# Kernel tuning notes

Hardware: AMD Instinct MI355X
Metric: run time of the kernel (lower is better)

Reference implementation:

```python
import jax, jax.numpy as jnp
import numpy as np

N = 50000   # nodes (single node type)
E = 200000  # edges per relation
R = 2       # relations (etypes)
D = 256     # in_dim == out_dim
H = 8       # heads
DK = D // H # 32
SQRT_DK = float(np.sqrt(DK))


def setup_inputs() -> dict:
    key = jax.random.key(0)
    ks = jax.random.split(key, 12)
    wsc = 1.0 / np.sqrt(D)   # linear-layer scale
    rsc = 1.0 / np.sqrt(DK)  # xavier-ish scale for relation tensors
    return {
        "x": jax.random.normal(ks[0], (N, D), jnp.float32),
        "src": jax.random.randint(ks[1], (R, E), 0, N, jnp.int32),
        "dst": jax.random.randint(ks[2], (R, E), 0, N, jnp.int32),
        "Wk": jax.random.normal(ks[3], (D, D), jnp.float32) * wsc,
        "bk": jnp.zeros((D,), jnp.float32),
        "Wq": jax.random.normal(ks[4], (D, D), jnp.float32) * wsc,
        "bq": jnp.zeros((D,), jnp.float32),
        "Wv": jax.random.normal(ks[5], (D, D), jnp.float32) * wsc,
        "bv": jnp.zeros((D,), jnp.float32),
        "Wa": jax.random.normal(ks[6], (D, D), jnp.float32) * wsc,
        "ba": jnp.zeros((D,), jnp.float32),
        "rel_pri": jnp.ones((R, H), jnp.float32),
        "rel_att": jax.random.normal(ks[7], (R, H, DK, DK), jnp.float32) * rsc,
        "rel_msg": jax.random.normal(ks[8], (R, H, DK, DK), jnp.float32) * rsc,
        "skip": jnp.ones((1,), jnp.float32),
    }


def reference(x, src, dst, Wk, bk, Wq, bq, Wv, bv, Wa, ba, rel_pri, rel_att, rel_msg, skip):
    # Per-type K/Q/V projections (single node type) -> [N,H,DK]
    k = (x @ Wk + bk).reshape(N, H, DK)
    q = (x @ Wq + bq).reshape(N, H, DK)
    v = (x @ Wv + bv).reshape(N, H, DK)

    # edge_attention: per-relation bmm transform of gathered src features
    key_t = jnp.einsum('rehd,rhdf->rehf', k[src], rel_att)   # [R,E,H,DK]
    val = jnp.einsum('rehd,rhdf->rehf', v[src], rel_msg)     # [R,E,H,DK]
    att = (q[dst] * key_t).sum(-1) * rel_pri[:, None, :] / SQRT_DK  # [R,E,H]

    # segment softmax over incoming edges per (relation, dst node)
    seg = (dst + N * jnp.arange(R, dtype=dst.dtype)[:, None]).reshape(-1)  # [R*E]
    att_f = att.reshape(R * E, H)
    m = jax.ops.segment_max(att_f, seg, num_segments=R * N)
    m = jnp.where(jnp.isfinite(m), m, 0.0)  # empty segments -> never gathered
    e = jnp.exp(att_f - m[seg])
    den = jax.ops.segment_sum(e, seg, num_segments=R * N)
    attn = e / den[seg]                                       # [R*E,H]

    # weighted-sum scatter aggregation, then cross_reducer='mean' over relations
    h = jax.ops.segment_sum(attn[:, :, None] * val.reshape(R * E, H, DK), seg,
                            num_segments=R * N)               # [R*N,H,DK]
    t = h.reshape(R, N, D).mean(axis=0)                        # [N,D]

    # skip-gated output projection (dropout inactive in eval, use_norm=False)
    alpha = jax.nn.sigmoid(skip[0])
    return (t @ Wa + ba) * alpha + x * (1.0 - alpha)
```

## Files before the change

kernel.cpp:

```cpp
#include <hip/hip_runtime.h>
#include <hip/hip_bf16.h>
#include <math.h>

#define NN 50000
#define EE 200000
#define DD 256
#define HH 8
#define DKK 32
#define NSEG (2 * NN)
#define SCAN_BLOCKS ((NSEG + 1023) / 1024)
#define MPAD 50048
#define LDQKV 1280

constexpr float RSQRT_DK = 0.17677669529663687f;

__device__ __forceinline__ float bf_lo(unsigned u) { return __uint_as_float(u << 16); }
__device__ __forceinline__ float bf_hi(unsigned u) { return __uint_as_float(u & 0xffff0000u); }
__device__ __forceinline__ unsigned short f2bf(float f) {
    unsigned u = __float_as_uint(f);
    return (unsigned short)((u + 0x7fffu + ((u >> 16) & 1u)) >> 16);
}

typedef __attribute__((ext_vector_type(8))) short bf16x8;
typedef __attribute__((ext_vector_type(4))) float f32x4;

#define GLDS16(g, l)                                                                   \
    __builtin_amdgcn_global_load_lds((const __attribute__((address_space(1))) unsigned int*)(g), \
                                     (__attribute__((address_space(3))) unsigned int*)(l), 16, 0, 0)

__global__ void cast_x_kernel(const float* __restrict__ x, unsigned short* __restrict__ xb) {
    const size_t i = ((size_t)blockIdx.x * 256 + threadIdx.x) * 4;
    float4 v = *(const float4*)&x[i];
    ushort4 o;
    o.x = f2bf(v.x); o.y = f2bf(v.y); o.z = f2bf(v.z); o.w = f2bf(v.w);
    *(ushort4*)&xb[i] = o;
}

__global__ void fold_qkv_kernel(const float* __restrict__ Wq, const float* __restrict__ Wk,
                                const float* __restrict__ Wv, const float* __restrict__ bq,
                                const float* __restrict__ bk, const float* __restrict__ bv,
                                const float* __restrict__ rel_att, const float* __restrict__ rel_msg,
                                unsigned short* __restrict__ Wt, float* __restrict__ bb) {
    const int n = blockIdx.x, kk = threadIdx.x;
    if (n < 256) {
        Wt[(size_t)n * 256 + kk] = f2bf(Wq[(size_t)kk * 256 + n]);
        if (kk == 0) bb[n] = bq[n];
        return;
    }
    const int sec = (n - 256) >> 8;
    const int c = (n - 256) & 255;
    const int h = c >> 5, f = c & 31;
    const float* W    = (sec < 2) ? Wk : Wv;
    const float* bsrc = (sec < 2) ? bk : bv;
    const float* T = ((sec < 2) ? rel_att : rel_msg)
                   + (size_t)(sec & 1) * HH * DKK * DKK + (size_t)h * DKK * DKK + f;
    const float* wrow = &W[(size_t)kk * 256 + h * 32];
    float s = 0.f;
    #pragma unroll
    for (int d = 0; d < 32; ++d) s += wrow[d] * T[(size_t)d * 32];
    Wt[(size_t)n * 256 + kk] = f2bf(s);
    if (kk == 0) {
        float sb = 0.f;
        for (int d = 0; d < 32; ++d) sb += bsrc[h * 32 + d] * T[(size_t)d * 32];
        bb[n] = sb;
    }
}

__global__ void cast_wa_kernel(const float* __restrict__ Wa, unsigned short* __restrict__ Bt) {
    const int n = blockIdx.x, kk = threadIdx.x;
    Bt[(size_t)n * 256 + kk] = f2bf(Wa[(size_t)kk * 256 + n]);
}

__global__ __launch_bounds__(256) void mfma_gemm(
        const unsigned short* __restrict__ A, const unsigned short* __restrict__ Bt,
        const float* __restrict__ bias,
        unsigned short* __restrict__ Cbf, float* __restrict__ Cf,
        int M, int ldc, const float* __restrict__ xres, const float* __restrict__ skip) {
    __shared__ __align__(16) unsigned short As[3][8][64][8];
    __shared__ __align__(16) unsigned short Bs[3][8][64][8];
    const int t = threadIdx.x;
    const int w = t >> 6, l = t & 63;

    const int nwg = gridDim.x * gridDim.y;
    int lin = blockIdx.y * gridDim.x + blockIdx.x;
    {
        const int xcd = lin & 7, pos = lin >> 3;
        const int q = nwg >> 3, r = nwg & 7;
        lin = (xcd < r ? xcd * (q + 1) : r * (q + 1) + (xcd - r) * q) + pos;
    }
    const int n0 = (lin % gridDim.x) * 128;
    const int m0 = (lin / gridDim.x) * 128;
    const int wm = w & 1, wn = w >> 1;

    const int sr = l & 15, sq = l >> 4;
    const unsigned short* ga0 = A  + (size_t)(m0 + w * 16 + sr) * 256 + sq * 8;
    const unsigned short* ga1 = A  + (size_t)(m0 + (w + 4) * 16 + sr) * 256 + sq * 8;
    const unsigned short* gb0 = Bt + (size_t)(n0 + w * 16 + sr) * 256 + sq * 8;
    const unsigned short* gb1 = Bt + (size_t)(n0 + (w + 4) * 16 + sr) * 256 + sq * 8;

#define STAGE(buf, k0) do {                    \
        GLDS16(ga0 + (k0), &As[buf][w][0][0]); \
        GLDS16(ga1 + (k0), &As[buf][w + 4][0][0]); \
        GLDS16(gb0 + (k0), &Bs[buf][w][0][0]); \
        GLDS16(gb1 + (k0), &Bs[buf][w + 4][0][0]); } while (0)

    f32x4 acc[4][4];
    #pragma unroll
    for (int mi = 0; mi < 4; ++mi)
        #pragma unroll
        for (int ni = 0; ni < 4; ++ni) acc[mi][ni] = (f32x4){0.f, 0.f, 0.f, 0.f};

    STAGE(0, 0);
    STAGE(1, 32);
    #pragma unroll
    for (int it = 0; it < 8; ++it) {
        if (it < 7) { asm volatile("s_waitcnt vmcnt(4)" ::: "memory"); }
        else        { asm volatile("s_waitcnt vmcnt(0)" ::: "memory"); }
        __builtin_amdgcn_s_barrier();
        __builtin_amdgcn_sched_barrier(0);
        if (it < 6) {
            STAGE((it + 2) % 3, (it + 2) * 32);
        }
        const int b = it % 3;
        bf16x8 af[4], bfr[4];
        #pragma unroll
        for (int i = 0; i < 4; ++i) {
            af[i]  = *(const bf16x8*)&As[b][wm * 4 + i][l][0];
            bfr[i] = *(const bf16x8*)&Bs[b][wn * 4 + i][l][0];
        }
        #pragma unroll
        for (int mi = 0; mi < 4; ++mi)
            #pragma unroll
            for (int ni = 0; ni < 4; ++ni)
                acc[mi][ni] = __builtin_amdgcn_mfma_f32_16x16x32_bf16(af[mi], bfr[ni],
                                                                      acc[mi][ni], 0, 0, 0);
    }
    __syncthreads();

    unsigned short* ep = (w < 2) ? &As[0][0][0][0] : &Bs[0][0][0][0];
    ep += (w & 1) * 4096;
    const int q4 = l >> 4, c15 = l & 15;

    if (Cf == nullptr) {
        #pragma unroll
        for (int ni = 0; ni < 4; ++ni) {
            const float bcol = bias[n0 + wn * 64 + ni * 16 + c15];
            const int g = ni * 2 + (c15 >> 3);
            #pragma unroll
            for (int mi = 0; mi < 4; ++mi)
                #pragma unroll
                for (int p = 0; p < 4; ++p) {
                    const int row = mi * 16 + q4 * 4 + p;
                    ep[row * 64 + ((g ^ (row & 7)) << 3) + (c15 & 7)] =
                        f2bf(acc[mi][ni][p] + bcol);
                }
        }
        __syncthreads();
        const int rs = l >> 3, cc = l & 7;
        #pragma unroll
        for (int i = 0; i < 8; ++i) {
            const int rl = i * 8 + rs;
            const int row = m0 + wm * 64 + rl;
            if (row < M) {
                uint4 v = *(const uint4*)&ep[rl * 64 + ((cc ^ (rl & 7)) << 3)];
                *(uint4*)&Cbf[(size_t)row * (size_t)ldc + n0 + wn * 64 + cc * 8] = v;
            }
        }
    } else {
        const float alpha = 1.f / (1.f + __expf(-skip[0]));
        const float beta = 1.f - alpha;
        float* epf = (float*)ep;
        #pragma unroll
        for (int half = 0; half < 2; ++half) {
            __syncthreads();
            #pragma unroll
            for (int mi2 = 0; mi2 < 2; ++mi2) {
                const int mi = half * 2 + mi2;
                #pragma unroll
                for (int ni = 0; ni < 4; ++ni) {
                    const float bcol = bias[n0 + wn * 64 + ni * 16 + c15];
                    const int g = ni * 4 + (c15 >> 2);
                    #pragma unroll
                    for (int p = 0; p < 4; ++p) {
                        const int row = mi2 * 16 + q4 * 4 + p;
                        epf[row * 64 + ((g ^ (row & 7)) << 2) + (c15 & 3)] =
                            acc[mi][ni][p] + bcol;
                    }
                }
            }
            __syncthreads();
            const int cc = l & 15, rs = l >> 4;
            #pragma unroll
            for (int i = 0; i < 8; ++i) {
                const int rl = i * 4 + rs;
                const int row = m0 + wm * 64 + half * 32 + rl;
                if (row < M) {
                    const int col = n0 + wn * 64 + cc * 4;
                    float4 v = *(const float4*)&epf[rl * 64 + ((cc ^ (rl & 7)) << 2)];
                    float4 xr = *(const float4*)&xres[(size_t)row * 256 + col];
                    v.x = v.x * alpha + xr.x * beta;
                    v.y = v.y * alpha + xr.y * beta;
                    v.z = v.z * alpha + xr.z * beta;
                    v.w = v.w * alpha + xr.w * beta;
                    *(float4*)&Cf[(size_t)row * 256 + col] = v;
                }
            }
        }
    }
#undef STAGE
}

__global__ void count_kernel(const int* __restrict__ dst, int* __restrict__ cnt) {
    int e = blockIdx.x * 256 + threadIdx.x;
    if (e < 2 * EE) atomicAdd(&cnt[(e / EE) * NN + dst[e]], 1);
}

__global__ __launch_bounds__(1024) void scan_local_kernel(const int* __restrict__ cnt,
                                                          int* __restrict__ rowptr,
                                                          int* __restrict__ bsum) {
    __shared__ int sh[1024];
    const int t = threadIdx.x;
    const int idx = blockIdx.x * 1024 + t;
    const int c = (idx < NSEG) ? cnt[idx] : 0;
    sh[t] = c;
    __syncthreads();
    #pragma unroll
    for (int ofs = 1; ofs < 1024; ofs <<= 1) {
        int v = (t >= ofs) ? sh[t - ofs] : 0;
        __syncthreads();
        sh[t] += v;
        __syncthreads();
    }
    if (idx < NSEG) rowptr[idx] = sh[t] - c;
    if (t == 1023) bsum[blockIdx.x] = sh[1023];
}

__global__ void scan_bsum_kernel(int* __restrict__ bsum, int* __restrict__ rowptr) {
    __shared__ int sh[128];
    const int t = threadIdx.x;
    const int v = (t < SCAN_BLOCKS) ? bsum[t] : 0;
    sh[t] = v;
    __syncthreads();
    #pragma unroll
    for (int ofs = 1; ofs < 128; ofs <<= 1) {
        int u = (t >= ofs) ? sh[t - ofs] : 0;
        __syncthreads();
        sh[t] += u;
        __syncthreads();
    }
    if (t < SCAN_BLOCKS) bsum[t] = sh[t] - v;
    if (t == 127) rowptr[NSEG] = sh[127];
}

__global__ __launch_bounds__(1024) void scan_add_kernel(int* __restrict__ rowptr,
                                                        const int* __restrict__ bsum) {
    const int idx = blockIdx.x * 1024 + threadIdx.x;
    if (idx < NSEG) rowptr[idx] += bsum[blockIdx.x];
}

__global__ void scatter_kernel(const int* __restrict__ src, const int* __restrict__ dst,
                               int* __restrict__ cursor, int* __restrict__ csr_src,
                               int* __restrict__ csr_eid) {
    int e = blockIdx.x * 256 + threadIdx.x;
    if (e >= 2 * EE) return;
    int seg = (e / EE) * NN + dst[e];
    int pos = atomicAdd(&cursor[seg], 1);
    csr_src[pos] = src[e];
    csr_eid[pos] = e;
}

__global__ void edge_att_kernel(const unsigned short* __restrict__ qkv,
                                const int* __restrict__ src, const int* __restrict__ dst,
                                const float* __restrict__ pri,
                                float* __restrict__ expatt) {
    const int half = threadIdx.x >> 5;
    const int ll = threadIdx.x & 31;
    const int h = ll >> 2, quad = ll & 3;
    const int e = blockIdx.x * 8 + half;
    const int r = (e >= EE) ? 1 : 0;
    const int s = src[e], d_ = dst[e];
    const size_t off = (size_t)(h * 32 + quad * 8);

    uint4 a = *(const uint4*)&qkv[(size_t)d_ * LDQKV + off];
    uint4 b = *(const uint4*)&qkv[(size_t)s * LDQKV + 256 + r * 256 + off];
    float p = bf_lo(a.x) * bf_lo(b.x) + bf_hi(a.x) * bf_hi(b.x)
            + bf_lo(a.y) * bf_lo(b.y) + bf_hi(a.y) * bf_hi(b.y)
            + bf_lo(a.z) * bf_lo(b.z) + bf_hi(a.z) * bf_hi(b.z)
            + bf_lo(a.w) * bf_lo(b.w) + bf_hi(a.w) * bf_hi(b.w);
    p += __shfl_xor(p, 1);
    p += __shfl_xor(p, 2);
    if (quad == 0) {
        expatt[(size_t)e * HH + h] = __expf(p * pri[r * HH + h] * RSQRT_DK);
    }
}

__global__ void node_agg_kernel(const unsigned short* __restrict__ qkv,
                                const int* __restrict__ csr_src,
                                const int* __restrict__ csr_eid,
                                const int* __restrict__ rowptr,
                                const float* __restrict__ expatt,
                                unsigned short* __restrict__ tt_bf) {
    const int wave = threadIdx.x >> 6, lane = threadIdx.x & 63;
    const int n = blockIdx.x * 4 + wave;
    const int h = lane >> 3;
    const int off = lane * 4;

    float4 tot = make_float4(0.f, 0.f, 0.f, 0.f);
    #pragma unroll
    for (int r = 0; r < 2; ++r) {
        const int seg = r * NN + n;
        const int j0 = rowptr[seg], j1 = rowptr[seg + 1];
        float4 acc = make_float4(0.f, 0.f, 0.f, 0.f);
        float den = 0.f;
        for (int j = j0; j < j1; ++j) {
            const int s = csr_src[j];
            const int e = csr_eid[j];
            const float a = expatt[(size_t)e * HH + h];
            den += a;
            uint2 b = *(const uint2*)&qkv[(size_t)s * LDQKV + 768 + r * 256 + off];
            acc.x += a * bf_lo(b.x);
            acc.y += a * bf_hi(b.x);
            acc.z += a * bf_lo(b.y);
            acc.w += a * bf_hi(b.y);
        }
        const float wgt = (den > 0.f) ? 0.5f / den : 0.f;
        tot.x += acc.x * wgt; tot.y += acc.y * wgt;
        tot.z += acc.z * wgt; tot.w += acc.w * wgt;
    }
    ushort4 ob;
    ob.x = f2bf(tot.x); ob.y = f2bf(tot.y); ob.z = f2bf(tot.z); ob.w = f2bf(tot.w);
    *(ushort4*)&tt_bf[(size_t)n * 256 + off] = ob;
}

extern "C" void kernel_launch(void* const* d_in, const int* in_sizes, int n_in,
                              void* d_out, int out_size, void* d_ws, size_t ws_size,
                              hipStream_t stream) {
    const float* x       = (const float*)d_in[0];
    const int*   src     = (const int*)d_in[1];
    const int*   dst     = (const int*)d_in[2];
    const float* Wk      = (const float*)d_in[3];
    const float* bk      = (const float*)d_in[4];
    const float* Wq      = (const float*)d_in[5];
    const float* bq      = (const float*)d_in[6];
    const float* Wv      = (const float*)d_in[7];
    const float* bv      = (const float*)d_in[8];
    const float* Wa      = (const float*)d_in[9];
    const float* ba      = (const float*)d_in[10];
    const float* rel_pri = (const float*)d_in[11];
    const float* rel_att = (const float*)d_in[12];
    const float* rel_msg = (const float*)d_in[13];
    const float* skip    = (const float*)d_in[14];
    float* out = (float*)d_out;
    char* ws = (char*)d_ws;

    const size_t ND = (size_t)NN * DD;
    size_t off = 0;
    unsigned short* x_bf   = (unsigned short*)(ws + off); off += (size_t)MPAD * DD * 2;
    unsigned short* qkv_bf = (unsigned short*)(ws + off); off += (size_t)NN * LDQKV * 2;
    unsigned short* tt_bf  = (unsigned short*)(ws + off); off += (size_t)MPAD * DD * 2;
    float*          expatt = (float*)(ws + off);          off += (size_t)2 * EE * HH * 4;
    unsigned short* wqkv_t = (unsigned short*)(ws + off); off += (size_t)LDQKV * 256 * 2;
    unsigned short* wa_t   = (unsigned short*)(ws + off); off += (size_t)256 * 256 * 2;
    float*          bb     = (float*)(ws + off);          off += LDQKV * 4;
    int*            cnt    = (int*)(ws + off);            off += (size_t)NSEG * 4;
    int*            rowptr = (int*)(ws + off);            off += (size_t)(NSEG + 1) * 4;
    int*            cursor = (int*)(ws + off);            off += (size_t)NSEG * 4;
    int*            bsum   = (int*)(ws + off);            off += 128 * 4;
    int*            csr_src= (int*)(ws + off);            off += (size_t)2 * EE * 4;
    int*            csr_eid= (int*)(ws + off);            off += (size_t)2 * EE * 4;
    if (ws_size < off) return;

    cast_x_kernel<<<(int)(ND / 1024), 256, 0, stream>>>(x, x_bf);
    fold_qkv_kernel<<<LDQKV, 256, 0, stream>>>(Wq, Wk, Wv, bq, bk, bv,
                                               rel_att, rel_msg, wqkv_t, bb);
    cast_wa_kernel<<<256, 256, 0, stream>>>(Wa, wa_t);

    dim3 g_qkv(LDQKV / 128, MPAD / 128);
    mfma_gemm<<<g_qkv, 256, 0, stream>>>(x_bf, wqkv_t, bb, qkv_bf, nullptr,
                                         NN, LDQKV, nullptr, nullptr);

    hipMemsetAsync(cnt, 0, (size_t)NSEG * 4, stream);
    const int eg = (2 * EE + 255) / 256;
    count_kernel<<<eg, 256, 0, stream>>>(dst, cnt);
    scan_local_kernel<<<SCAN_BLOCKS, 1024, 0, stream>>>(cnt, rowptr, bsum);
    scan_bsum_kernel<<<1, 128, 0, stream>>>(bsum, rowptr);
    scan_add_kernel<<<SCAN_BLOCKS, 1024, 0, stream>>>(rowptr, bsum);
    hipMemcpyAsync(cursor, rowptr, (size_t)NSEG * 4, hipMemcpyDeviceToDevice, stream);
    scatter_kernel<<<eg, 256, 0, stream>>>(src, dst, cursor, csr_src, csr_eid);

    edge_att_kernel<<<2 * EE / 8, 256, 0, stream>>>(qkv_bf, src, dst, rel_pri, expatt);
    node_agg_kernel<<<NN / 4, 256, 0, stream>>>(qkv_bf, csr_src, csr_eid, rowptr,
                                                expatt, tt_bf);

    dim3 g_out(DD / 128, MPAD / 128);
    mfma_gemm<<<g_out, 256, 0, stream>>>(tt_bf, wa_t, ba, nullptr, out,
                                         NN, DD, x, skip);
}
```

Baseline: 427.7 us.

## Fuse edge attention scoring into CSR node aggregation and drop edge-id buffers

Removes the separate edge_att kernel and its expatt buffer. node_agg now loads the destination's q once, gathers k and v for each incoming edge, computes the head dot product with shuffles and exponentiates it inline. The csr_eid array is no longer needed, and the cursor copy is folded into scan_add, removing a memcpy. This cuts one launch plus the edge-score write and read traffic, in exchange for more serial per-edge work inside the aggregation loop.

```diff
diff --git a/kernel.cpp b/kernel.cpp
--- a/kernel.cpp
+++ b/kernel.cpp
@@ -253,75 +253,64 @@
 }
 
 __global__ __launch_bounds__(1024) void scan_add_kernel(int* __restrict__ rowptr,
-                                                        const int* __restrict__ bsum) {
+                                                        const int* __restrict__ bsum,
+                                                        int* __restrict__ cursor) {
     const int idx = blockIdx.x * 1024 + threadIdx.x;
-    if (idx < NSEG) rowptr[idx] += bsum[blockIdx.x];
+    if (idx < NSEG) {
+        const int v = rowptr[idx] + bsum[blockIdx.x];
+        rowptr[idx] = v;
+        cursor[idx] = v;
+    }
 }
 
 __global__ void scatter_kernel(const int* __restrict__ src, const int* __restrict__ dst,
-                               int* __restrict__ cursor, int* __restrict__ csr_src,
-                               int* __restrict__ csr_eid) {
+                               int* __restrict__ cursor, int* __restrict__ csr_src) {
     int e = blockIdx.x * 256 + threadIdx.x;
     if (e >= 2 * EE) return;
     int seg = (e / EE) * NN + dst[e];
     int pos = atomicAdd(&cursor[seg], 1);
     csr_src[pos] = src[e];
-    csr_eid[pos] = e;
-}
-
-__global__ void edge_att_kernel(const unsigned short* __restrict__ qkv,
-                                const int* __restrict__ src, const int* __restrict__ dst,
-                                const float* __restrict__ pri,
-                                float* __restrict__ expatt) {
-    const int half = threadIdx.x >> 5;
-    const int ll = threadIdx.x & 31;
-    const int h = ll >> 2, quad = ll & 3;
-    const int e = blockIdx.x * 8 + half;
-    const int r = (e >= EE) ? 1 : 0;
-    const int s = src[e], d_ = dst[e];
-    const size_t off = (size_t)(h * 32 + quad * 8);
-
-    uint4 a = *(const uint4*)&qkv[(size_t)d_ * LDQKV + off];
-    uint4 b = *(const uint4*)&qkv[(size_t)s * LDQKV + 256 + r * 256 + off];
-    float p = bf_lo(a.x) * bf_lo(b.x) + bf_hi(a.x) * bf_hi(b.x)
-            + bf_lo(a.y) * bf_lo(b.y) + bf_hi(a.y) * bf_hi(b.y)
-            + bf_lo(a.z) * bf_lo(b.z) + bf_hi(a.z) * bf_hi(b.z)
-            + bf_lo(a.w) * bf_lo(b.w) + bf_hi(a.w) * bf_hi(b.w);
-    p += __shfl_xor(p, 1);
-    p += __shfl_xor(p, 2);
-    if (quad == 0) {
-        expatt[(size_t)e * HH + h] = __expf(p * pri[r * HH + h] * RSQRT_DK);
-    }
 }
 
 __global__ void node_agg_kernel(const unsigned short* __restrict__ qkv,
                                 const int* __restrict__ csr_src,
-                                const int* __restrict__ csr_eid,
                                 const int* __restrict__ rowptr,
-                                const float* __restrict__ expatt,
+                                const float* __restrict__ pri,
                                 unsigned short* __restrict__ tt_bf) {
     const int wave = threadIdx.x >> 6, lane = threadIdx.x & 63;
     const int n = blockIdx.x * 4 + wave;
     const int h = lane >> 3;
     const int off = lane * 4;
 
+    const uint2 qv = *(const uint2*)&qkv[(size_t)n * LDQKV + off];
+    const float q0 = bf_lo(qv.x), q1 = bf_hi(qv.x), q2 = bf_lo(qv.y), q3 = bf_hi(qv.y);
+
     float4 tot = make_float4(0.f, 0.f, 0.f, 0.f);
     #pragma unroll
     for (int r = 0; r < 2; ++r) {
+        const float prm = pri[r * HH + h] * RSQRT_DK;
         const int seg = r * NN + n;
         const int j0 = rowptr[seg], j1 = rowptr[seg + 1];
+        const size_t kbase = 256 + (size_t)r * 256 + off;
+        const size_t vbase = 768 + (size_t)r * 256 + off;
         float4 acc = make_float4(0.f, 0.f, 0.f, 0.f);
         float den = 0.f;
         for (int j = j0; j < j1; ++j) {
             const int s = csr_src[j];
-            const int e = csr_eid[j];
-            const float a = expatt[(size_t)e * HH + h];
+            const size_t rowb = (size_t)s * LDQKV;
+            const uint2 kv = *(const uint2*)&qkv[rowb + kbase];
+            const uint2 vv = *(const uint2*)&qkv[rowb + vbase];
+            float p = q0 * bf_lo(kv.x) + q1 * bf_hi(kv.x)
+                    + q2 * bf_lo(kv.y) + q3 * bf_hi(kv.y);
+            p += __shfl_xor(p, 1);
+            p += __shfl_xor(p, 2);
+            p += __shfl_xor(p, 4);
+            const float a = __expf(p * prm);
             den += a;
-            uint2 b = *(const uint2*)&qkv[(size_t)s * LDQKV + 768 + r * 256 + off];
-            acc.x += a * bf_lo(b.x);
-            acc.y += a * bf_hi(b.x);
-            acc.z += a * bf_lo(b.y);
-            acc.w += a * bf_hi(b.y);
+            acc.x += a * bf_lo(vv.x);
+            acc.y += a * bf_hi(vv.x);
+            acc.z += a * bf_lo(vv.y);
+            acc.w += a * bf_hi(vv.y);
         }
         const float wgt = (den > 0.f) ? 0.5f / den : 0.f;
         tot.x += acc.x * wgt; tot.y += acc.y * wgt;
@@ -358,7 +347,6 @@
     unsigned short* x_bf   = (unsigned short*)(ws + off); off += (size_t)MPAD * DD * 2;
     unsigned short* qkv_bf = (unsigned short*)(ws + off); off += (size_t)NN * LDQKV * 2;
     unsigned short* tt_bf  = (unsigned short*)(ws + off); off += (size_t)MPAD * DD * 2;
-    float*          expatt = (float*)(ws + off);          off += (size_t)2 * EE * HH * 4;
     unsigned short* wqkv_t = (unsigned short*)(ws + off); off += (size_t)LDQKV * 256 * 2;
     unsigned short* wa_t   = (unsigned short*)(ws + off); off += (size_t)256 * 256 * 2;
     float*          bb     = (float*)(ws + off);          off += LDQKV * 4;
@@ -367,7 +355,6 @@
     int*            cursor = (int*)(ws + off);            off += (size_t)NSEG * 4;
     int*            bsum   = (int*)(ws + off);            off += 128 * 4;
     int*            csr_src= (int*)(ws + off);            off += (size_t)2 * EE * 4;
-    int*            csr_eid= (int*)(ws + off);            off += (size_t)2 * EE * 4;
     if (ws_size < off) return;
 
     cast_x_kernel<<<(int)(ND / 1024), 256, 0, stream>>>(x, x_bf);
@@ -384,13 +371,11 @@
     count_kernel<<<eg, 256, 0, stream>>>(dst, cnt);
     scan_local_kernel<<<SCAN_BLOCKS, 1024, 0, stream>>>(cnt, rowptr, bsum);
     scan_bsum_kernel<<<1, 128, 0, stream>>>(bsum, rowptr);
-    scan_add_kernel<<<SCAN_BLOCKS, 1024, 0, stream>>>(rowptr, bsum);
-    hipMemcpyAsync(cursor, rowptr, (size_t)NSEG * 4, hipMemcpyDeviceToDevice, stream);
-    scatter_kernel<<<eg, 256, 0, stream>>>(src, dst, cursor, csr_src, csr_eid);
-
-    edge_att_kernel<<<2 * EE / 8, 256, 0, stream>>>(qkv_bf, src, dst, rel_pri, expatt);
-    node_agg_kernel<<<NN / 4, 256, 0, stream>>>(qkv_bf, csr_src, csr_eid, rowptr,
-                                                expatt, tt_bf);
+    scan_add_kernel<<<SCAN_BLOCKS, 1024, 0, stream>>>(rowptr, bsum, cursor);
+    scatter_kernel<<<eg, 256, 0, stream>>>(src, dst, cursor, csr_src);
+
+    node_agg_kernel<<<NN / 4, 256, 0, stream>>>(qkv_bf, csr_src, rowptr,
+                                                rel_pri, tt_bf);
 
     dim3 g_out(DD / 128, MPAD / 128);
     mfma_gemm<<<g_out, 256, 0, stream>>>(tt_bf, wa_t, ba, nullptr, out,
```

Result: faster. 377.2 us (-11.8%).
